# Kernel tuning notes

Hardware: AMD Instinct MI355X
Metric: run time of the kernel (lower is better)

The kernel has to match this reference:

```python
import jax, jax.numpy as jnp
import numpy as np

N_NODES = 100000
N_EDGES = 600000
N_GRAPHS = 2000
H = 128
L = 3
EPS = 1e-5


def layer_norm(x, g, b):
    m = jnp.mean(x, axis=-1, keepdims=True)
    v = jnp.mean((x - m) ** 2, axis=-1, keepdims=True)
    return (x - m) / jnp.sqrt(v + EPS) * g + b


def setup_inputs() -> dict:
    key = jax.random.key(0)
    ks = jax.random.split(key, 32)
    s = 0.05
    d = {}
    d['atom_features'] = jax.random.normal(ks[0], (N_NODES, 4), jnp.float32)
    d['edge_index'] = jax.random.randint(ks[1], (2, N_EDGES), 0, N_NODES, jnp.int32)
    d['edge_attr'] = jax.random.uniform(ks[2], (N_EDGES, 1), jnp.float32)
    d['batch'] = jnp.sort(jax.random.randint(ks[3], (N_NODES,), 0, N_GRAPHS, jnp.int32))
    # atom encoder
    d['enc_w'] = jax.random.normal(ks[4], (4, H)) * s
    d['enc_b'] = jnp.zeros((H,))
    d['enc_ln_g'] = jnp.ones((H,))
    d['enc_ln_b'] = jnp.zeros((H,))
    # stacked per-layer MPNN params (L layers)
    d['msg_w1'] = jax.random.normal(ks[5], (L, 2 * H + 1, 2 * H)) * s
    d['msg_b1'] = jnp.zeros((L, 2 * H))
    d['msg_w2'] = jax.random.normal(ks[6], (L, 2 * H, H)) * s
    d['msg_b2'] = jnp.zeros((L, H))
    d['gru_wih'] = jax.random.normal(ks[7], (L, 3 * H, H)) * s
    d['gru_whh'] = jax.random.normal(ks[8], (L, 3 * H, H)) * s
    d['gru_bih'] = jnp.zeros((L, 3 * H))
    d['gru_bhh'] = jnp.zeros((L, 3 * H))
    d['ln_g'] = jnp.ones((L, H))
    d['ln_b'] = jnp.zeros((L, H))
    # readout MLP (dropout is eval-mode identity)
    d['ro_w1'] = jax.random.normal(ks[9], (2 * H, H)) * s
    d['ro_b1'] = jnp.zeros((H,))
    d['ro_w2'] = jax.random.normal(ks[10], (H, H // 2)) * s
    d['ro_b2'] = jnp.zeros((H // 2,))
    d['ro_w3'] = jax.random.normal(ks[11], (H // 2, 113)) * s
    d['ro_b3'] = jnp.zeros((113,))
    return d


def _forward(atom_features, edge_attr, enc_w, enc_b, enc_ln_g, enc_ln_b,
             msg_w1, msg_b1, msg_w2, msg_b2, gru_wih, gru_whh, gru_bih, gru_bhh,
             ln_g, ln_b, ro_w1, ro_b1, ro_w2, ro_b2, ro_w3, ro_b3,
             edge_index, batch):
    n = atom_features.shape[0]
    x = layer_norm(jax.nn.relu(atom_features @ enc_w + enc_b), enc_ln_g, enc_ln_b)
    src, dst = edge_index[0], edge_index[1]
    for l in range(L):
        # gather-concat-MLP messages: [E, 2H+1] -> [E, 2H] -> [E, H]
        m = jnp.concatenate([x[src], x[dst], edge_attr], axis=-1)
        m = jax.nn.relu(m @ msg_w1[l] + msg_b1[l]) @ msg_w2[l] + msg_b2[l]
        aggr = jax.ops.segment_sum(m, dst, num_segments=n)  # index_add
        # GRUCell(input=aggr, hidden=x)
        gi = aggr @ gru_wih[l].T + gru_bih[l]
        gh = x @ gru_whh[l].T + gru_bhh[l]
        i_r, i_z, i_n = jnp.split(gi, 3, axis=-1)
        h_r, h_z, h_n = jnp.split(gh, 3, axis=-1)
        r = jax.nn.sigmoid(i_r + h_r)
        z = jax.nn.sigmoid(i_z + h_z)
        nn_ = jnp.tanh(i_n + r * h_n)
        x_new = (1.0 - z) * nn_ + z * x
        x = layer_norm(x + x_new, ln_g[l], ln_b[l])
    # per-graph mean+max pooling
    ones = jnp.ones((n,), x.dtype)
    counts = jax.ops.segment_sum(ones, batch, num_segments=N_GRAPHS)
    mean_pool = jax.ops.segment_sum(x, batch, num_segments=N_GRAPHS) / jnp.maximum(counts, 1.0)[:, None]
    max_pool = jax.ops.segment_max(x, batch, num_segments=N_GRAPHS)
    g = jnp.concatenate([mean_pool, max_pool], axis=-1)  # [B, 2H]
    h1 = jax.nn.relu(g @ ro_w1 + ro_b1)
    h2 = jax.nn.relu(h1 @ ro_w2 + ro_b2)
    return h2 @ ro_w3 + ro_b3  # [B, 113]


def reference(atom_features, edge_index, edge_attr, batch, enc_w, enc_b, enc_ln_g, enc_ln_b,
              msg_w1, msg_b1, msg_w2, msg_b2, gru_wih, gru_whh, gru_bih, gru_bhh,
              ln_g, ln_b, ro_w1, ro_b1, ro_w2, ro_b2, ro_w3, ro_b3):
    return _forward(atom_features, edge_attr, enc_w, enc_b, enc_ln_g, enc_ln_b,
                    msg_w1, msg_b1, msg_w2, msg_b2, gru_wih, gru_whh, gru_bih, gru_bhh,
                    ln_g, ln_b, ro_w1, ro_b1, ro_w2, ro_b2, ro_w3, ro_b3,
                    edge_index, batch)
```

## Files before the change

### kernel.cpp

```cpp
#include <hip/hip_runtime.h>
#include <hip/hip_bf16.h>
#include <math.h>

#define NN 100000
#define NE_TOT 600000
#define NG 2000
#define HD 128
#define NL 3
#define LN_EPS 1e-5f

typedef __attribute__((ext_vector_type(8))) short short8;
typedef __attribute__((ext_vector_type(4))) float f32x4;

__device__ __forceinline__ unsigned short f2bf(float f){
  union { float f; unsigned int u; } x; x.f = f;
  unsigned int r = (x.u + 0x7FFFu + ((x.u >> 16) & 1u)) >> 16;
  return (unsigned short)r;
}
__device__ __forceinline__ float bf2f(unsigned short u){
  union { unsigned int i; float f; } x; x.i = ((unsigned int)u) << 16; return x.f;
}

__device__ __forceinline__ float wave_sum64(float v){
  #pragma unroll
  for (int o = 32; o > 0; o >>= 1) v += __shfl_xor(v, o, 64);
  return v;
}

__global__ __launch_bounds__(256) void k_zero4(float4* p, int n4){
  int i = blockIdx.x * 256 + threadIdx.x;
  if (i < n4) p[i] = make_float4(0.f, 0.f, 0.f, 0.f);
}

__global__ __launch_bounds__(256) void k_hist(const int* __restrict__ ei, int* __restrict__ cnt){
  int e = blockIdx.x * 256 + threadIdx.x;
  if (e < NE_TOT) atomicAdd(&cnt[ei[NE_TOT + e]], 1);
}

__global__ __launch_bounds__(1024) void k_scan1(const int* __restrict__ cnt,
                                                int* __restrict__ loc,
                                                int* __restrict__ bsum){
  __shared__ int w_s[16];
  int t = threadIdx.x, lane = t & 63, wv = t >> 6;
  int g = blockIdx.x * 1024 + t;
  int v = (g < NN) ? cnt[g] : 0;
  int s = v;
  #pragma unroll
  for (int o = 1; o < 64; o <<= 1){
    int u = __shfl_up(s, o, 64);
    if (lane >= o) s += u;
  }
  if (lane == 63) w_s[wv] = s;
  __syncthreads();
  if (t == 0){
    int run = 0;
    #pragma unroll
    for (int i = 0; i < 16; ++i){ int c = w_s[i]; w_s[i] = run; run += c; }
    bsum[blockIdx.x] = run;
  }
  __syncthreads();
  if (g < NN) loc[g] = s - v + w_s[wv];
}

__global__ __launch_bounds__(128) void k_scan2(const int* __restrict__ bsum,
                                               int* __restrict__ bscan){
  __shared__ int w0_s;
  int t = threadIdx.x, lane = t & 63, wv = t >> 6;
  int v = (t < 98) ? bsum[t] : 0;
  int s = v;
  #pragma unroll
  for (int o = 1; o < 64; o <<= 1){
    int u = __shfl_up(s, o, 64);
    if (lane >= o) s += u;
  }
  if (wv == 0 && lane == 63) w0_s = s;
  __syncthreads();
  if (wv == 1) s += w0_s;
  if (t < 98) bscan[t] = s - v;
}

__global__ __launch_bounds__(1024) void k_scan3(const int* __restrict__ loc,
                                                const int* __restrict__ bscan,
                                                int* __restrict__ cur){
  int g = blockIdx.x * 1024 + threadIdx.x;
  if (g < NN) cur[g] = loc[g] + bscan[blockIdx.x];
}

__global__ __launch_bounds__(256) void k_scatter(const int* __restrict__ ei,
    const float* __restrict__ eattr, int* __restrict__ cur,
    int* __restrict__ srcs, int* __restrict__ dsts, float* __restrict__ attrs){
  int e = blockIdx.x * 256 + threadIdx.x;
  if (e >= NE_TOT) return;
  int d = ei[NE_TOT + e];
  int p = atomicAdd(&cur[d], 1);
  srcs[p] = ei[e];
  dsts[p] = d;
  attrs[p] = eattr[e];
}

#define GW_LPL 102400
#define GW_O2  67584
#define GW_O3  84992
__global__ __launch_bounds__(256) void k_gprep(const float* __restrict__ wih,
                                               const float* __restrict__ whh,
                                               unsigned short* __restrict__ gw){
  int idx = blockIdx.x * 256 + threadIdx.x;
  if (idx >= 2 * 3 * 384 * 128) return;
  int which = (idx >= 3 * 384 * 128);
  int i = which ? idx - 3 * 384 * 128 : idx;
  int l = i / 49152;
  int r = i - l * 49152;
  int j = r >> 7, k = r & 127;
  float v = which ? whh[i] : wih[i];
  size_t o;
  if (!which){
    o = (j < 256) ? ((size_t)l * GW_LPL + (size_t)j * 264 + k)
                  : ((size_t)l * GW_LPL + GW_O2 + (size_t)(j - 256) * 136 + k);
  } else {
    o = (j < 256) ? ((size_t)l * GW_LPL + (size_t)j * 264 + 128 + k)
                  : ((size_t)l * GW_LPL + GW_O3 + (size_t)(j - 256) * 136 + k);
  }
  gw[o] = f2bf(v);
}

#define W1N_LS (512 * 136)
__global__ __launch_bounds__(256) void k_mprep(const float* __restrict__ w1,
                                               unsigned short* __restrict__ w1n){
  int idx = blockIdx.x * 256 + threadIdx.x;
  if (idx >= 3 * 512 * 128) return;
  int l = idx / (512 * 128);
  int r = idx - l * (512 * 128);
  int j = r >> 7, k = r & 127;
  const float* wl = w1 + (size_t)l * 257 * 256;
  float v = (j < 256) ? wl[k * 256 + j] : wl[(128 + k) * 256 + (j - 256)];
  w1n[(size_t)l * W1N_LS + j * 136 + k] = f2bf(v);
}

#define W2T_LS (128 * 264)
__global__ __launch_bounds__(256) void k_w2prep(const float* __restrict__ w2,
                                                unsigned short* __restrict__ w2T){
  int idx = blockIdx.x * 256 + threadIdx.x;
  if (idx >= 3 * 128 * 256) return;
  int l = idx >> 15;
  int r = idx & 32767;
  int c = r >> 8, k = r & 255;
  w2T[(size_t)l * W2T_LS + c * 264 + k] = f2bf(w2[(size_t)l * 256 * 128 + k * 128 + c]);
}

__global__ __launch_bounds__(256) void k_enc(const float* __restrict__ af,
    const float* __restrict__ w, const float* __restrict__ b,
    const float* __restrict__ lg, const float* __restrict__ lb,
    unsigned short* __restrict__ xbf){
  int wv = threadIdx.x >> 6, lane = threadIdx.x & 63;
  int n = blockIdx.x * 4 + wv;
  float4 a = *reinterpret_cast<const float4*>(af + (size_t)n * 4);
  int c0 = lane, c1 = lane + 64;
  float v0 = fmaf(a.x, w[c0], fmaf(a.y, w[128 + c0], fmaf(a.z, w[256 + c0], fmaf(a.w, w[384 + c0], b[c0]))));
  float v1 = fmaf(a.x, w[c1], fmaf(a.y, w[128 + c1], fmaf(a.z, w[256 + c1], fmaf(a.w, w[384 + c1], b[c1]))));
  v0 = fmaxf(v0, 0.f); v1 = fmaxf(v1, 0.f);
  float m = wave_sum64(v0 + v1) * (1.f / 128.f);
  float d0 = v0 - m, d1 = v1 - m;
  float var = wave_sum64(d0 * d0 + d1 * d1) * (1.f / 128.f);
  float rstd = rsqrtf(var + LN_EPS);
  xbf[(size_t)n * HD + c0] = f2bf(d0 * rstd * lg[c0] + lb[c0]);
  xbf[(size_t)n * HD + c1] = f2bf(d1 * rstd * lg[c1] + lb[c1]);
}

__global__ __launch_bounds__(256, 2) void k_ngemm(const unsigned short* __restrict__ xbf,
    const unsigned short* __restrict__ w1n, const float* __restrict__ b1,
    unsigned short* __restrict__ gsd, float* __restrict__ aggr){
  int tid = threadIdx.x, lane = tid & 63, wv = tid >> 6;
  int r16 = lane & 15, kg = lane >> 4;
  {
    int nrow = NN - blockIdx.x * 64; if (nrow > 64) nrow = 64;
    float4* az = (float4*)(aggr + (size_t)blockIdx.x * 64 * HD);
    int n4 = nrow * (HD / 4);
    for (int i = tid; i < n4; i += 256) az[i] = make_float4(0.f, 0.f, 0.f, 0.f);
  }
  int n = blockIdx.x * 64 + wv * 16 + r16;
  int nc = (n < NN) ? n : NN - 1;
  short8 bfr[4];
  #pragma unroll
  for (int k0 = 0; k0 < 4; ++k0)
    bfr[k0] = *reinterpret_cast<const short8*>(xbf + (size_t)nc * HD + k0 * 32 + kg * 8);
  f32x4 acc[32];
  #pragma unroll
  for (int it = 0; it < 32; ++it) acc[it] = (f32x4){0.f, 0.f, 0.f, 0.f};
  #pragma unroll
  for (int it = 0; it < 32; ++it){
    const unsigned short* ap = w1n + (size_t)(it * 16 + r16) * 136 + kg * 8;
    #pragma unroll
    for (int k0 = 0; k0 < 4; ++k0){
      short8 af = *reinterpret_cast<const short8*>(ap + k0 * 32);
      acc[it] = __builtin_amdgcn_mfma_f32_16x16x32_bf16(af, bfr[k0], acc[it], 0, 0, 0);
    }
  }
  if (n < NN){
    #pragma unroll
    for (int it = 0; it < 32; ++it){
      int c0 = it * 16 + kg * 4;
      ushort4 h;
      float v0 = acc[it][0], v1 = acc[it][1], v2 = acc[it][2], v3 = acc[it][3];
      if (c0 >= 256){
        v0 += b1[c0 - 256]; v1 += b1[c0 - 255]; v2 += b1[c0 - 254]; v3 += b1[c0 - 253];
      }
      h.x = f2bf(v0); h.y = f2bf(v1); h.z = f2bf(v2); h.w = f2bf(v3);
      *reinterpret_cast<ushort4*>(gsd + (size_t)n * 512 + c0) = h;
    }
  }
}

#define EBM 64
__global__ __launch_bounds__(256, 4) void k_msg(const unsigned short* __restrict__ gsd,
    const int* __restrict__ srcs, const int* __restrict__ dsts,
    const float* __restrict__ attrs, const float* __restrict__ w1attr,
    const unsigned short* __restrict__ w2T, const float* __restrict__ b2,
    float* __restrict__ aggr){
  __shared__ __align__(16) unsigned char smem[33280];
  unsigned short* h_s = (unsigned short*)smem;
  float* scr = (float*)smem;
  __shared__ float w1a_s[256];
  __shared__ float b2_s[128];
  __shared__ int   dst_s[EBM];
  __shared__ float attr_s[EBM];
  int tid = threadIdx.x;
  int lane = tid & 63, wv = tid >> 6;
  int r16 = lane & 15, kg = lane >> 4;
  int ebase = blockIdx.x * EBM;

  w1a_s[tid] = w1attr[tid & 255];
  if (tid < 128) b2_s[tid] = b2[tid];
  if (tid < EBM){ dst_s[tid] = dsts[ebase + tid]; attr_s[tid] = attrs[ebase + tid]; }
  __syncthreads();

  {
    int e = tid >> 2, q = tid & 3;
    int sn = srcs[ebase + e];
    int dn = dst_s[e];
    float at = attr_s[e];
    const unsigned short* gp = gsd + (size_t)sn * 512;
    const unsigned short* dp = gsd + (size_t)dn * 512 + 256;
    #pragma unroll
    for (int j8 = 0; j8 < 8; ++j8){
      int colb = j8 * 32 + q * 8;
      short8 gv = *reinterpret_cast<const short8*>(gp + colb);
      short8 dv = *reinterpret_cast<const short8*>(dp + colb);
      unsigned short hh[8];
      #pragma unroll
      for (int i = 0; i < 8; ++i){
        float v = bf2f((unsigned short)gv[i]) + bf2f((unsigned short)dv[i]) + at * w1a_s[colb + i];
        hh[i] = f2bf(fmaxf(v, 0.f));
      }
      int slot = colb >> 3;
      int slotw = (slot & ~7) | ((slot ^ e) & 7);
      *reinterpret_cast<int4*>(&h_s[e * 256 + slotw * 8]) = *reinterpret_cast<int4*>(hh);
    }
  }
  __syncthreads();

  f32x4 acc2[4][2];
  #pragma unroll
  for (int rt = 0; rt < 4; ++rt)
    #pragma unroll
    for (int ct = 0; ct < 2; ++ct)
      acc2[rt][ct] = (f32x4){0.f, 0.f, 0.f, 0.f};
  int cbase2 = wv * 32;
  {
    short8 a[4], bb[2];
    const unsigned short* w2b = w2T + (size_t)(cbase2 + r16) * 264 + kg * 8;
    for (int k0 = 0; k0 < 8; ++k0){
      #pragma unroll
      for (int rt = 0; rt < 4; ++rt){
        int row = rt * 16 + r16;
        int slot = k0 * 4 + kg;
        int slotw = (slot & ~7) | ((slot ^ row) & 7);
        a[rt] = *reinterpret_cast<const short8*>(&h_s[row * 256 + slotw * 8]);
      }
      #pragma unroll
      for (int ct = 0; ct < 2; ++ct)
        bb[ct] = *reinterpret_cast<const short8*>(w2b + ct * 16 * 264 + k0 * 32);
      #pragma unroll
      for (int rt = 0; rt < 4; ++rt)
        #pragma unroll
        for (int ct = 0; ct < 2; ++ct)
          acc2[rt][ct] = __builtin_amdgcn_mfma_f32_16x16x32_bf16(a[rt], bb[ct], acc2[rt][ct], 0, 0, 0);
    }
  }
  __syncthreads();

  #pragma unroll
  for (int ct = 0; ct < 2; ++ct){
    int col = cbase2 + ct * 16 + r16;
    #pragma unroll
    for (int rt = 0; rt < 4; ++rt){
      #pragma unroll
      for (int r = 0; r < 4; ++r){
        int row = rt * 16 + kg * 4 + r;
        scr[row * 130 + col] = acc2[rt][ct][r];
      }
    }
  }
  __syncthreads();

  {
    int c = tid & 127, h = tid >> 7;
    int r0 = h * 32;
    float bias = b2_s[c];
    int pd = dst_s[r0];
    float acc = scr[r0 * 130 + c] + bias;
    #pragma unroll 4
    for (int r = 1; r < 32; ++r){
      int row = r0 + r;
      float v = scr[row * 130 + c] + bias;
      int d = dst_s[row];
      if (d != pd){
        atomicAdd(&aggr[(size_t)pd * HD + c], acc);
        acc = v; pd = d;
      } else {
        acc += v;
      }
    }
    atomicAdd(&aggr[(size_t)pd * HD + c], acc);
  }
}

#define GRB 64
__global__ __launch_bounds__(256, 2) void k_gru(unsigned short* __restrict__ xbf,
    const float* __restrict__ aggr,
    const unsigned short* __restrict__ gw,
    const float* __restrict__ bih, const float* __restrict__ bhh,
    const float* __restrict__ lg, const float* __restrict__ lb){
  __shared__ unsigned short a_s[GRB * 256];
  __shared__ float psum[GRB][2][2];
  int tid = threadIdx.x;
  int lane = tid & 63, wv = tid >> 6;
  int r16 = lane & 15, kg = lane >> 4;
  int rg = wv >> 1, cg = wv & 1;
  int nbase = blockIdx.x * GRB;

  {
    int row = tid >> 2, qc = (tid & 3) * 32;
    int n = nbase + row; if (n >= NN) n = NN - 1;
    const float* ap = aggr + (size_t)n * HD + qc;
    #pragma unroll
    for (int j = 0; j < 8; ++j){
      float4 v = *reinterpret_cast<const float4*>(ap + j * 4);
      ushort4 h;
      h.x = f2bf(v.x); h.y = f2bf(v.y); h.z = f2bf(v.z); h.w = f2bf(v.w);
      int col = qc + j * 4;
      int slot = col >> 3;
      int slotw = (slot & ~7) | ((slot ^ row) & 7);
      *reinterpret_cast<ushort4*>(&a_s[row * 256 + slotw * 8 + (col & 7)]) = h;
    }
  }
  {
    int row = tid >> 2, q = tid & 3;
    int n = nbase + row; if (n >= NN) n = NN - 1;
    const unsigned short* xp = xbf + (size_t)n * HD + q * 32;
    #pragma unroll
    for (int j = 0; j < 4; ++j){
      int4 v = *reinterpret_cast<const int4*>(xp + j * 8);
      int col = 128 + q * 32 + j * 8;
      int slot = col >> 3;
      int slotw = (slot & ~7) | ((slot ^ row) & 7);
      *reinterpret_cast<int4*>(&a_s[row * 256 + slotw * 8]) = v;
    }
  }
  __syncthreads();

  short8 a[2][8];
  #pragma unroll
  for (int rt = 0; rt < 2; ++rt){
    int arow = rg * 32 + rt * 16 + r16;
    #pragma unroll
    for (int k0 = 0; k0 < 8; ++k0){
      int slot = k0 * 4 + kg;
      int slotw = (slot & ~7) | ((slot ^ arow) & 7);
      a[rt][k0] = *reinterpret_cast<const short8*>(&a_s[arow * 256 + slotw * 8]);
    }
  }

  f32x4 accR[2][4], accZ[2][4], accI[2][4], accH[2][4];
  #pragma unroll
  for (int rt = 0; rt < 2; ++rt)
    #pragma unroll
    for (int ct = 0; ct < 4; ++ct){
      accR[rt][ct] = (f32x4){0.f, 0.f, 0.f, 0.f};
      accZ[rt][ct] = (f32x4){0.f, 0.f, 0.f, 0.f};
      accI[rt][ct] = (f32x4){0.f, 0.f, 0.f, 0.f};
      accH[rt][ct] = (f32x4){0.f, 0.f, 0.f, 0.f};
    }

  int jb = cg * 64;
  #pragma unroll
  for (int ct = 0; ct < 4; ++ct){
    const unsigned short* bpR = gw + (size_t)(jb + ct * 16 + r16) * 264 + kg * 8;
    const unsigned short* bpZ = gw + (size_t)(128 + jb + ct * 16 + r16) * 264 + kg * 8;
    #pragma unroll
    for (int k0 = 0; k0 < 8; ++k0){
      short8 bR = *reinterpret_cast<const short8*>(bpR + k0 * 32);
      accR[0][ct] = __builtin_amdgcn_mfma_f32_16x16x32_bf16(a[0][k0], bR, accR[0][ct], 0, 0, 0);
      accR[1][ct] = __builtin_amdgcn_mfma_f32_16x16x32_bf16(a[1][k0], bR, accR[1][ct], 0, 0, 0);
      short8 bZ = *reinterpret_cast<const short8*>(bpZ + k0 * 32);
      accZ[0][ct] = __builtin_amdgcn_mfma_f32_16x16x32_bf16(a[0][k0], bZ, accZ[0][ct], 0, 0, 0);
      accZ[1][ct] = __builtin_amdgcn_mfma_f32_16x16x32_bf16(a[1][k0], bZ, accZ[1][ct], 0, 0, 0);
    }
    const unsigned short* bpI = gw + GW_O2 + (size_t)(jb + ct * 16 + r16) * 136 + kg * 8;
    const unsigned short* bpH = gw + GW_O3 + (size_t)(jb + ct * 16 + r16) * 136 + kg * 8;
    #pragma unroll
    for (int k0 = 0; k0 < 4; ++k0){
      short8 bI = *reinterpret_cast<const short8*>(bpI + k0 * 32);
      accI[0][ct] = __builtin_amdgcn_mfma_f32_16x16x32_bf16(a[0][k0], bI, accI[0][ct], 0, 0, 0);
      accI[1][ct] = __builtin_amdgcn_mfma_f32_16x16x32_bf16(a[1][k0], bI, accI[1][ct], 0, 0, 0);
      short8 bH = *reinterpret_cast<const short8*>(bpH + k0 * 32);
      accH[0][ct] = __builtin_amdgcn_mfma_f32_16x16x32_bf16(a[0][k0 + 4], bH, accH[0][ct], 0, 0, 0);
      accH[1][ct] = __builtin_amdgcn_mfma_f32_16x16x32_bf16(a[1][k0 + 4], bH, accH[1][ct], 0, 0, 0);
    }
  }

  #pragma unroll
  for (int rt = 0; rt < 2; ++rt){
    #pragma unroll
    for (int ct = 0; ct < 4; ++ct){
      int j = jb + ct * 16 + r16;
      float br = bih[j] + bhh[j];
      float bz = bih[j + 128] + bhh[j + 128];
      float bin = bih[j + 256], bhn = bhh[j + 256];
      #pragma unroll
      for (int r = 0; r < 4; ++r){
        int n = nbase + rg * 32 + rt * 16 + kg * 4 + r;
        int nc = (n < NN) ? n : NN - 1;
        float xv = bf2f(xbf[(size_t)nc * HD + j]);
        float rgt = accR[rt][ct][r] + br;  rgt = 1.f / (1.f + __expf(-rgt));
        float zg  = accZ[rt][ct][r] + bz;  zg  = 1.f / (1.f + __expf(-zg));
        float ng  = tanhf(accI[rt][ct][r] + bin + rgt * (accH[rt][ct][r] + bhn));
        accR[rt][ct][r] = xv + (1.f - zg) * ng + zg * xv;
      }
    }
  }

  #pragma unroll
  for (int rt = 0; rt < 2; ++rt){
    #pragma unroll
    for (int r = 0; r < 4; ++r){
      float s = 0.f, q = 0.f;
      #pragma unroll
      for (int ct = 0; ct < 4; ++ct){ float v = accR[rt][ct][r]; s += v; q += v * v; }
      #pragma unroll
      for (int o = 1; o <= 8; o <<= 1){ s += __shfl_xor(s, o, 64); q += __shfl_xor(q, o, 64); }
      if (r16 == 0){
        int l = rg * 32 + rt * 16 + kg * 4 + r;
        psum[l][cg][0] = s;
        psum[l][cg][1] = q;
      }
    }
  }
  __syncthreads();

  #pragma unroll
  for (int rt = 0; rt < 2; ++rt){
    #pragma unroll
    for (int r = 0; r < 4; ++r){
      int l = rg * 32 + rt * 16 + kg * 4 + r;
      float S = psum[l][0][0] + psum[l][1][0];
      float Q = psum[l][0][1] + psum[l][1][1];
      float m = S * (1.f / 128.f);
      float var = Q * (1.f / 128.f) - m * m;
      float rstd = rsqrtf(fmaxf(var, 0.f) + LN_EPS);
      int n = nbase + rg * 32 + rt * 16 + kg * 4 + r;
      if (n < NN){
        #pragma unroll
        for (int ct = 0; ct < 4; ++ct){
          int j = jb + ct * 16 + r16;
          xbf[(size_t)n * HD + j] = f2bf((accR[rt][ct][r] - m) * rstd * lg[j] + lb[j]);
        }
      }
    }
  }
}

__device__ __forceinline__ int lowerb(const int* __restrict__ a, int v){
  int lo = 0, hi = NN;
  while (lo < hi){ int mid = (lo + hi) >> 1; if (a[mid] < v) lo = mid + 1; else hi = mid; }
  return lo;
}

__global__ __launch_bounds__(128) void k_pool(const unsigned short* __restrict__ xbf,
    const int* __restrict__ batch,
    const float* __restrict__ w1, const float* __restrict__ b1,
    const float* __restrict__ w2, const float* __restrict__ b2,
    const float* __restrict__ w3, const float* __restrict__ b3,
    float* __restrict__ out){
  __shared__ float g_s[256];
  __shared__ float h1_s[128];
  __shared__ float h2_s[64];
  int g = blockIdx.x, tid = threadIdx.x;
  int s = lowerb(batch, g), t = lowerb(batch, g + 1);
  float sum = 0.f, mx = -INFINITY;
  for (int n = s; n < t; ++n){
    float v = bf2f(xbf[(size_t)n * HD + tid]);
    sum += v; mx = fmaxf(mx, v);
  }
  int cnt = t - s;
  g_s[tid]       = sum / fmaxf((float)cnt, 1.f);
  g_s[tid + 128] = (cnt > 0) ? mx : -INFINITY;
  __syncthreads();
  float a1 = b1[tid];
  for (int k = 0; k < 256; ++k) a1 = fmaf(g_s[k], w1[k * 128 + tid], a1);
  h1_s[tid] = fmaxf(a1, 0.f);
  __syncthreads();
  if (tid < 64){
    float a2 = b2[tid];
    for (int k = 0; k < 128; ++k) a2 = fmaf(h1_s[k], w2[k * 64 + tid], a2);
    h2_s[tid] = fmaxf(a2, 0.f);
  }
  __syncthreads();
  if (tid < 113){
    float a3 = b3[tid];
    for (int k = 0; k < 64; ++k) a3 = fmaf(h2_s[k], w3[k * 113 + tid], a3);
    out[(size_t)g * 113 + tid] = a3;
  }
}

extern "C" void kernel_launch(void* const* d_in, const int* in_sizes, int n_in,
                              void* d_out, int out_size, void* d_ws, size_t ws_size,
                              hipStream_t stream){
  (void)in_sizes; (void)n_in; (void)out_size; (void)ws_size;
  const float* af     = (const float*)d_in[0];
  const int*   ei     = (const int*)  d_in[1];
  const float* eattr  = (const float*)d_in[2];
  const int*   batch  = (const int*)  d_in[3];
  const float* enc_w  = (const float*)d_in[4];
  const float* enc_b  = (const float*)d_in[5];
  const float* enc_lg = (const float*)d_in[6];
  const float* enc_lb = (const float*)d_in[7];
  const float* mw1    = (const float*)d_in[8];
  const float* mb1    = (const float*)d_in[9];
  const float* mw2    = (const float*)d_in[10];
  const float* mb2    = (const float*)d_in[11];
  const float* gwih   = (const float*)d_in[12];
  const float* gwhh   = (const float*)d_in[13];
  const float* gbih   = (const float*)d_in[14];
  const float* gbhh   = (const float*)d_in[15];
  const float* lng    = (const float*)d_in[16];
  const float* lnb    = (const float*)d_in[17];
  const float* rw1    = (const float*)d_in[18];
  const float* rb1    = (const float*)d_in[19];
  const float* rw2    = (const float*)d_in[20];
  const float* rb2    = (const float*)d_in[21];
  const float* rw3    = (const float*)d_in[22];
  const float* rb3    = (const float*)d_in[23];
  float* out = (float*)d_out;
  char* ws = (char*)d_ws;

  size_t off = 0;
  auto carve = [&](size_t bytes)->char*{
    char* p = ws + off;
    off = (off + bytes + 255) & ~(size_t)255;
    return p;
  };
  unsigned short* xbf  = (unsigned short*)carve((size_t)NN * HD * 2);
  float*          aggr = (float*)         carve((size_t)NN * HD * 4);
  unsigned short* gsd  = (unsigned short*)carve((size_t)NN * 512 * 2);
  unsigned short* gw   = (unsigned short*)carve((size_t)3 * GW_LPL * 2);
  unsigned short* w1n  = (unsigned short*)carve((size_t)3 * W1N_LS * 2);
  unsigned short* w2T  = (unsigned short*)carve((size_t)3 * W2T_LS * 2);
  int*   cnt   = (int*)  carve((size_t)NN * 4);
  int*   cur   = (int*)  carve((size_t)NN * 4);
  int*   loc   = (int*)  carve((size_t)NN * 4);
  int*   bsum  = (int*)  carve((size_t)128 * 4);
  int*   bscan = (int*)  carve((size_t)128 * 4);
  int*   srcs  = (int*)  carve((size_t)NE_TOT * 4);
  int*   dsts  = (int*)  carve((size_t)NE_TOT * 4);
  float* attrs = (float*)carve((size_t)NE_TOT * 4);

  k_zero4<<<(NN / 4 + 255) / 256, 256, 0, stream>>>((float4*)cnt, NN / 4);
  k_hist<<<(NE_TOT + 255) / 256, 256, 0, stream>>>(ei, cnt);
  k_scan1<<<98, 1024, 0, stream>>>(cnt, loc, bsum);
  k_scan2<<<1, 128, 0, stream>>>(bsum, bscan);
  k_scan3<<<98, 1024, 0, stream>>>(loc, bscan, cur);
  k_scatter<<<(NE_TOT + 255) / 256, 256, 0, stream>>>(ei, eattr, cur, srcs, dsts, attrs);
  k_gprep<<<1152, 256, 0, stream>>>(gwih, gwhh, gw);
  k_mprep<<<768, 256, 0, stream>>>(mw1, w1n);
  k_w2prep<<<384, 256, 0, stream>>>(mw2, w2T);
  k_enc<<<NN / 4, 256, 0, stream>>>(af, enc_w, enc_b, enc_lg, enc_lb, xbf);

  for (int l = 0; l < NL; ++l){
    k_ngemm<<<(NN + 63) / 64, 256, 0, stream>>>(xbf,
        w1n + (size_t)l * W1N_LS, mb1 + (size_t)l * 256, gsd, aggr);
    k_msg<<<NE_TOT / EBM, 256, 0, stream>>>(gsd, srcs, dsts, attrs,
        mw1 + (size_t)l * 257 * 256 + 256 * 256,
        w2T + (size_t)l * W2T_LS, mb2 + (size_t)l * 128, aggr);
    k_gru<<<(NN + GRB - 1) / GRB, 256, 0, stream>>>(xbf, aggr,
        gw + (size_t)l * GW_LPL,
        gbih + (size_t)l * 384, gbhh + (size_t)l * 384,
        lng + (size_t)l * HD, lnb + (size_t)l * HD);
  }
  k_pool<<<NG, 128, 0, stream>>>(xbf, batch, rw1, rb1, rw2, rb2, rw3, rb3, out);
}
```

Before: 1.008 ms.

## Keep message hidden fragments in registers and give each wave 16 edges

The message kernel is reorganized so each wave owns 16 edges and builds the MFMA A-operand fragments directly in registers from the gathered bf16 node projections. This removes the shared-memory staging of the hidden activations and two barriers. Each wave now computes all 128 output columns, streaming W2 from global/L1 instead of sharing A tiles across waves. The edge-attribute weight row is pre-converted to bf16 in the prep kernel, which slightly lowers its precision. The output scratch uses an XOR swizzle in place of padding. Register pressure rises from holding 16 gathered vectors plus 8 fragments, and per-wave W2 loads grow.

```diff
diff --git a/kernel.cpp b/kernel.cpp
--- a/kernel.cpp
+++ b/kernel.cpp
@@ -138,13 +138,21 @@
 
 #define W2T_LS (128 * 264)
 __global__ __launch_bounds__(256) void k_w2prep(const float* __restrict__ w2,
-                                                unsigned short* __restrict__ w2T){
+                                                const float* __restrict__ w1,
+                                                unsigned short* __restrict__ w2T,
+                                                unsigned short* __restrict__ w1ab){
   int idx = blockIdx.x * 256 + threadIdx.x;
-  if (idx >= 3 * 128 * 256) return;
-  int l = idx >> 15;
-  int r = idx & 32767;
-  int c = r >> 8, k = r & 255;
-  w2T[(size_t)l * W2T_LS + c * 264 + k] = f2bf(w2[(size_t)l * 256 * 128 + k * 128 + c]);
+  const int T = 3 * 128 * 256;
+  if (idx < T){
+    int l = idx >> 15;
+    int r = idx & 32767;
+    int c = r >> 8, k = r & 255;
+    w2T[(size_t)l * W2T_LS + c * 264 + k] = f2bf(w2[(size_t)l * 256 * 128 + k * 128 + c]);
+  } else if (idx < T + 3 * 256){
+    int i2 = idx - T;
+    int l = i2 >> 8, c = i2 & 255;
+    w1ab[l * 256 + c] = f2bf(w1[(size_t)l * 257 * 256 + 256 * 256 + c]);
+  }
 }
 
 __global__ __launch_bounds__(256) void k_enc(const float* __restrict__ af,
@@ -213,91 +221,70 @@
 #define EBM 64
 __global__ __launch_bounds__(256, 4) void k_msg(const unsigned short* __restrict__ gsd,
     const int* __restrict__ srcs, const int* __restrict__ dsts,
-    const float* __restrict__ attrs, const float* __restrict__ w1attr,
+    const float* __restrict__ attrs, const unsigned short* __restrict__ w1ab,
     const unsigned short* __restrict__ w2T, const float* __restrict__ b2,
     float* __restrict__ aggr){
-  __shared__ __align__(16) unsigned char smem[33280];
-  unsigned short* h_s = (unsigned short*)smem;
-  float* scr = (float*)smem;
-  __shared__ float w1a_s[256];
-  __shared__ float b2_s[128];
-  __shared__ int   dst_s[EBM];
-  __shared__ float attr_s[EBM];
+  __shared__ float scr[EBM * 128];
+  __shared__ int dst_s[EBM];
   int tid = threadIdx.x;
   int lane = tid & 63, wv = tid >> 6;
   int r16 = lane & 15, kg = lane >> 4;
   int ebase = blockIdx.x * EBM;
 
-  w1a_s[tid] = w1attr[tid & 255];
-  if (tid < 128) b2_s[tid] = b2[tid];
-  if (tid < EBM){ dst_s[tid] = dsts[ebase + tid]; attr_s[tid] = attrs[ebase + tid]; }
-  __syncthreads();
-
+  if (tid < EBM) dst_s[tid] = dsts[ebase + tid];
+
+  int e = ebase + wv * 16 + r16;
+  int sn = srcs[e];
+  int dn = dsts[e];
+  float at = attrs[e];
+
+  short8 gv[8], dv[8];
   {
-    int e = tid >> 2, q = tid & 3;
-    int sn = srcs[ebase + e];
-    int dn = dst_s[e];
-    float at = attr_s[e];
-    const unsigned short* gp = gsd + (size_t)sn * 512;
-    const unsigned short* dp = gsd + (size_t)dn * 512 + 256;
+    const unsigned short* gp = gsd + (size_t)sn * 512 + kg * 8;
+    const unsigned short* dp = gsd + (size_t)dn * 512 + 256 + kg * 8;
     #pragma unroll
     for (int j8 = 0; j8 < 8; ++j8){
-      int colb = j8 * 32 + q * 8;
-      short8 gv = *reinterpret_cast<const short8*>(gp + colb);
-      short8 dv = *reinterpret_cast<const short8*>(dp + colb);
-      unsigned short hh[8];
+      gv[j8] = *reinterpret_cast<const short8*>(gp + j8 * 32);
+      dv[j8] = *reinterpret_cast<const short8*>(dp + j8 * 32);
+    }
+  }
+  short8 hfrag[8];
+  #pragma unroll
+  for (int j8 = 0; j8 < 8; ++j8){
+    short8 wa = *reinterpret_cast<const short8*>(w1ab + j8 * 32 + kg * 8);
+    unsigned short hh[8];
+    #pragma unroll
+    for (int i = 0; i < 8; ++i){
+      float v = bf2f((unsigned short)gv[j8][i]) + bf2f((unsigned short)dv[j8][i])
+              + at * bf2f((unsigned short)wa[i]);
+      hh[i] = f2bf(fmaxf(v, 0.f));
+    }
+    hfrag[j8] = *reinterpret_cast<short8*>(hh);
+  }
+
+  f32x4 acc[8];
+  #pragma unroll
+  for (int t = 0; t < 8; ++t) acc[t] = (f32x4){0.f, 0.f, 0.f, 0.f};
+  {
+    const unsigned short* w2b = w2T + (size_t)r16 * 264 + kg * 8;
+    #pragma unroll
+    for (int t = 0; t < 8; ++t){
+      const unsigned short* bp = w2b + (size_t)t * 16 * 264;
       #pragma unroll
-      for (int i = 0; i < 8; ++i){
-        float v = bf2f((unsigned short)gv[i]) + bf2f((unsigned short)dv[i]) + at * w1a_s[colb + i];
-        hh[i] = f2bf(fmaxf(v, 0.f));
+      for (int step = 0; step < 8; ++step){
+        short8 b = *reinterpret_cast<const short8*>(bp + step * 32);
+        acc[t] = __builtin_amdgcn_mfma_f32_16x16x32_bf16(hfrag[step], b, acc[t], 0, 0, 0);
       }
-      int slot = colb >> 3;
-      int slotw = (slot & ~7) | ((slot ^ e) & 7);
-      *reinterpret_cast<int4*>(&h_s[e * 256 + slotw * 8]) = *reinterpret_cast<int4*>(hh);
-    }
-  }
-  __syncthreads();
-
-  f32x4 acc2[4][2];
-  #pragma unroll
-  for (int rt = 0; rt < 4; ++rt)
-    #pragma unroll
-    for (int ct = 0; ct < 2; ++ct)
-      acc2[rt][ct] = (f32x4){0.f, 0.f, 0.f, 0.f};
-  int cbase2 = wv * 32;
-  {
-    short8 a[4], bb[2];
-    const unsigned short* w2b = w2T + (size_t)(cbase2 + r16) * 264 + kg * 8;
-    for (int k0 = 0; k0 < 8; ++k0){
-      #pragma unroll
-      for (int rt = 0; rt < 4; ++rt){
-        int row = rt * 16 + r16;
-        int slot = k0 * 4 + kg;
-        int slotw = (slot & ~7) | ((slot ^ row) & 7);
-        a[rt] = *reinterpret_cast<const short8*>(&h_s[row * 256 + slotw * 8]);
-      }
-      #pragma unroll
-      for (int ct = 0; ct < 2; ++ct)
-        bb[ct] = *reinterpret_cast<const short8*>(w2b + ct * 16 * 264 + k0 * 32);
-      #pragma unroll
-      for (int rt = 0; rt < 4; ++rt)
-        #pragma unroll
-        for (int ct = 0; ct < 2; ++ct)
-          acc2[rt][ct] = __builtin_amdgcn_mfma_f32_16x16x32_bf16(a[rt], bb[ct], acc2[rt][ct], 0, 0, 0);
-    }
-  }
-  __syncthreads();
-
-  #pragma unroll
-  for (int ct = 0; ct < 2; ++ct){
-    int col = cbase2 + ct * 16 + r16;
-    #pragma unroll
-    for (int rt = 0; rt < 4; ++rt){
-      #pragma unroll
-      for (int r = 0; r < 4; ++r){
-        int row = rt * 16 + kg * 4 + r;
-        scr[row * 130 + col] = acc2[rt][ct][r];
-      }
+    }
+  }
+
+  #pragma unroll
+  for (int t = 0; t < 8; ++t){
+    #pragma unroll
+    for (int r = 0; r < 4; ++r){
+      int er = wv * 16 + kg * 4 + r;
+      int col = t * 16 + r16;
+      scr[er * 128 + (col ^ ((er & 7) << 2))] = acc[t][r];
     }
   }
   __syncthreads();
@@ -305,22 +292,22 @@
   {
     int c = tid & 127, h = tid >> 7;
     int r0 = h * 32;
-    float bias = b2_s[c];
+    float bias = b2[c];
     int pd = dst_s[r0];
-    float acc = scr[r0 * 130 + c] + bias;
+    float a = scr[r0 * 128 + (c ^ ((r0 & 7) << 2))] + bias;
     #pragma unroll 4
     for (int r = 1; r < 32; ++r){
       int row = r0 + r;
-      float v = scr[row * 130 + c] + bias;
+      float v = scr[row * 128 + (c ^ ((row & 7) << 2))] + bias;
       int d = dst_s[row];
       if (d != pd){
-        atomicAdd(&aggr[(size_t)pd * HD + c], acc);
-        acc = v; pd = d;
+        atomicAdd(&aggr[(size_t)pd * HD + c], a);
+        a = v; pd = d;
       } else {
-        acc += v;
+        a += v;
       }
     }
-    atomicAdd(&aggr[(size_t)pd * HD + c], acc);
+    atomicAdd(&aggr[(size_t)pd * HD + c], a);
   }
 }
 
@@ -565,6 +552,7 @@
   unsigned short* gw   = (unsigned short*)carve((size_t)3 * GW_LPL * 2);
   unsigned short* w1n  = (unsigned short*)carve((size_t)3 * W1N_LS * 2);
   unsigned short* w2T  = (unsigned short*)carve((size_t)3 * W2T_LS * 2);
+  unsigned short* w1ab = (unsigned short*)carve((size_t)3 * 256 * 2);
   int*   cnt   = (int*)  carve((size_t)NN * 4);
   int*   cur   = (int*)  carve((size_t)NN * 4);
   int*   loc   = (int*)  carve((size_t)NN * 4);
@@ -582,14 +570,14 @@
   k_scatter<<<(NE_TOT + 255) / 256, 256, 0, stream>>>(ei, eattr, cur, srcs, dsts, attrs);
   k_gprep<<<1152, 256, 0, stream>>>(gwih, gwhh, gw);
   k_mprep<<<768, 256, 0, stream>>>(mw1, w1n);
-  k_w2prep<<<384, 256, 0, stream>>>(mw2, w2T);
+  k_w2prep<<<387, 256, 0, stream>>>(mw2, mw1, w2T, w1ab);
   k_enc<<<NN / 4, 256, 0, stream>>>(af, enc_w, enc_b, enc_lg, enc_lb, xbf);
 
   for (int l = 0; l < NL; ++l){
     k_ngemm<<<(NN + 63) / 64, 256, 0, stream>>>(xbf,
         w1n + (size_t)l * W1N_LS, mb1 + (size_t)l * 256, gsd, aggr);
     k_msg<<<NE_TOT / EBM, 256, 0, stream>>>(gsd, srcs, dsts, attrs,
-        mw1 + (size_t)l * 257 * 256 + 256 * 256,
+        w1ab + (size_t)l * 256,
         w2T + (size_t)l * W2T_LS, mb2 + (size_t)l * 128, aggr);
     k_gru<<<(NN + GRB - 1) / GRB, 256, 0, stream>>>(xbf, aggr,
         gw + (size_t)l * GW_LPL,
```

New measurement: 1.248 ms. 23.7% more time.
